# Performance work log

Hardware: AMD Instinct MI355X
Metric: run time of the kernel (lower is better)

## Reference

```python
import jax, jax.numpy as jnp
import numpy as np

G, N_NODES, E, H, D, IN_DIM, NS = 1024, 64, 128, 8, 32, 256, 48
EPS = 1e-6

def setup_inputs() -> dict:
    key = jax.random.key(0)
    ks = jax.random.split(key, 10)
    s = 1.0 / np.sqrt(IN_DIM)
    return {
        'h': jax.random.normal(ks[0], (G * N_NODES, IN_DIM), jnp.float32),
        'Wq': jax.random.normal(ks[1], (IN_DIM, H * D), jnp.float32) * s,
        'bq': jax.random.normal(ks[2], (H * D,), jnp.float32) * 0.01,
        'Wk': jax.random.normal(ks[3], (IN_DIM, H * D), jnp.float32) * s,
        'bk': jax.random.normal(ks[4], (H * D,), jnp.float32) * 0.01,
        'Wv': jax.random.normal(ks[5], (IN_DIM, H * D), jnp.float32) * s,
        'bv': jax.random.normal(ks[6], (H * D,), jnp.float32) * 0.01,
        'src': jax.random.randint(ks[7], (E,), 0, N_NODES, jnp.int32),
        'dst': jax.random.randint(ks[8], (E,), 0, N_NODES, jnp.int32),
        'ns': jax.random.randint(ks[9], (E, NS), 0, N_NODES, jnp.int32),
    }

def reference(h, Wq, bq, Wk, bk, Wv, bv, src, dst, ns):
    # per-node projections, reshaped per-graph: [G, n, H, D]
    Q = (h @ Wq + bq).reshape(G, N_NODES, H, D)
    K = (h @ Wk + bk).reshape(G, N_NODES, H, D)
    V = (h @ Wv + bv).reshape(G, N_NODES, H, D)
    # QK[g, s, h, t] = Q[g,s,h] . K[g,t,h], clamped as in torch .clamp(-5, 5)
    QK = jnp.clip(jnp.einsum('gshd,gthd->gsht', Q, K), -5.0, 5.0)  # [G, n, H, n]
    QKs = QK[:, src]  # rows for each edge's source node: [G, E, H, n]
    # numerator: QK[:, src_e, :, dst_e]
    num = jnp.take_along_axis(
        QKs, jnp.broadcast_to(dst[None, :, None, None].astype(jnp.int32), (G, E, H, 1)), axis=3
    )[..., 0]  # [G, E, H]
    # denominator: sum of QK[:, src_e, :, non_siblings(e)]
    den = jnp.take_along_axis(
        QKs, jnp.broadcast_to(ns[None, :, None, :], (G, E, H, NS)), axis=3
    ).sum(-1)  # [G, E, H]
    score = num / (den + EPS)  # [G, E, H]
    # scatter-sum aggregation: wV[g, dst] += V[g, src] * score; z[g, dst] += score
    msg = V[:, src] * score[..., None]  # [G, E, H, D]
    seg = (jnp.arange(G, dtype=jnp.int32)[:, None] * N_NODES + dst[None, :]).reshape(-1)
    wV = jax.ops.segment_sum(msg.reshape(G * E, H, D), seg, num_segments=G * N_NODES)
    z = jax.ops.segment_sum(score.reshape(G * E, H), seg, num_segments=G * N_NODES)
    return wV / (z[..., None] + EPS)  # [G*n, H, D]
```

## Files before the change

kernel.cpp:

```cpp
#include <hip/hip_runtime.h>

#define NG    1024
#define NN    64
#define NE    128
#define NH    8
#define ND    32
#define INDIM 256
#define NS_   48
#define EPS_  1e-6
#define BK    16

#define WS_QKV_FLOATS ((size_t)NG * NH * 3 * NN * ND)
#define WS_ELIST_OFF  (WS_QKV_FLOATS * sizeof(float))
#define WS_CNT_OFF    (WS_ELIST_OFF + (size_t)NN * 64 * sizeof(unsigned short))
#define WS_NEED2      (WS_CNT_OFF + (size_t)NN * sizeof(int))

__global__ __launch_bounds__(256, 2) void qkv_gemm_kernel(
    const float* __restrict__ h,
    const float* __restrict__ Wq, const float* __restrict__ bq,
    const float* __restrict__ Wk, const float* __restrict__ bk,
    const float* __restrict__ Wv, const float* __restrict__ bv,
    float* __restrict__ ws)
{
  const int b    = blockIdx.x;
  const int xcd  = b & 7;
  const int slot = b >> 3;
  const int rt   = xcd * 64 + slot / 3;
  const int sel  = slot % 3;
  const int tid  = threadIdx.x;

  const float* W  = (sel == 0) ? Wq : (sel == 1) ? Wk : Wv;
  const float* bs = (sel == 0) ? bq : (sel == 1) ? bk : bv;

  __shared__ float hT[BK][132];
  __shared__ float wT[BK][260];

  const int ty  = tid >> 5;
  const int tx  = tid & 31;
  const int r16 = ty * 16;
  const int ca  = tx * 4;
  const int cb  = 128 + tx * 4;

  float acc[16][8];
  #pragma unroll
  for (int i = 0; i < 16; ++i)
    #pragma unroll
    for (int j = 0; j < 8; ++j) acc[i][j] = 0.f;

  const int ra  = tid >> 1;
  const int kof = (tid & 1) * 8;
  const int kb2 = tid >> 6;
  const int c4  = (tid & 63) * 4;
  const float* hp0 = h + ((size_t)(rt * 128 + ra)) * INDIM + kof;
  const float* wp0 = W + (size_t)kb2 * (NH * ND) + c4;

  float4 pa0, pa1, pb[4];
  pa0 = *(const float4*)(hp0);
  pa1 = *(const float4*)(hp0 + 4);
  #pragma unroll
  for (int j = 0; j < 4; ++j)
    pb[j] = *(const float4*)(wp0 + (size_t)(4 * j) * (NH * ND));

  for (int kc = 0; kc < INDIM / BK; ++kc) {
    __syncthreads();
    hT[kof + 0][ra] = pa0.x; hT[kof + 1][ra] = pa0.y;
    hT[kof + 2][ra] = pa0.z; hT[kof + 3][ra] = pa0.w;
    hT[kof + 4][ra] = pa1.x; hT[kof + 5][ra] = pa1.y;
    hT[kof + 6][ra] = pa1.z; hT[kof + 7][ra] = pa1.w;
    #pragma unroll
    for (int j = 0; j < 4; ++j)
      *(float4*)&wT[kb2 + 4 * j][c4] = pb[j];
    __syncthreads();

    if (kc + 1 < INDIM / BK) {
      const int k0n = (kc + 1) * BK;
      pa0 = *(const float4*)(hp0 + k0n);
      pa1 = *(const float4*)(hp0 + k0n + 4);
      #pragma unroll
      for (int j = 0; j < 4; ++j)
        pb[j] = *(const float4*)(wp0 + (size_t)(k0n + 4 * j) * (NH * ND));
    }

    #pragma unroll
    for (int k = 0; k < BK; ++k) {
      float4 a0 = *(const float4*)&hT[k][r16];
      float4 a1 = *(const float4*)&hT[k][r16 + 4];
      float4 a2 = *(const float4*)&hT[k][r16 + 8];
      float4 a3 = *(const float4*)&hT[k][r16 + 12];
      float4 b0 = *(const float4*)&wT[k][ca];
      float4 b1 = *(const float4*)&wT[k][cb];
      const float av[16] = {a0.x,a0.y,a0.z,a0.w, a1.x,a1.y,a1.z,a1.w,
                            a2.x,a2.y,a2.z,a2.w, a3.x,a3.y,a3.z,a3.w};
      #pragma unroll
      for (int i = 0; i < 16; ++i) {
        acc[i][0] += av[i] * b0.x;
        acc[i][1] += av[i] * b0.y;
        acc[i][2] += av[i] * b0.z;
        acc[i][3] += av[i] * b0.w;
        acc[i][4] += av[i] * b1.x;
        acc[i][5] += av[i] * b1.y;
        acc[i][6] += av[i] * b1.z;
        acc[i][7] += av[i] * b1.w;
      }
    }
  }

  const int hda = ca >> 5, d0a = ca & 31;
  const int hdb = cb >> 5, d0b = cb & 31;
  float ba4[4], bb4[4];
  #pragma unroll
  for (int j = 0; j < 4; ++j) { ba4[j] = bs[ca + j]; bb4[j] = bs[cb + j]; }

  #pragma unroll
  for (int i = 0; i < 16; ++i) {
    const int r = rt * 128 + r16 + i;
    const int g = r >> 6, n = r & 63;
    float* opa = ws + ((((size_t)(g * NH + hda)) * 3 + sel) * NN + n) * ND + d0a;
    float* opb = ws + ((((size_t)(g * NH + hdb)) * 3 + sel) * NN + n) * ND + d0b;
    *(float4*)opa = make_float4(acc[i][0] + ba4[0], acc[i][1] + ba4[1],
                                acc[i][2] + ba4[2], acc[i][3] + ba4[3]);
    *(float4*)opb = make_float4(acc[i][4] + bb4[0], acc[i][5] + bb4[1],
                                acc[i][6] + bb4[2], acc[i][7] + bb4[3]);
  }
}

__global__ void edge_setup_kernel(const int* __restrict__ dst,
                                  unsigned short* __restrict__ elist,
                                  int* __restrict__ cnt)
{
  const int n = threadIdx.x;
  if (n < NN) {
    int c = 0;
    for (int e = 0; e < NE; ++e) {
      if (dst[e] == n) {
        if (c < 64) elist[n * 64 + c] = (unsigned short)e;
        ++c;
      }
    }
    cnt[n] = (c > 64) ? 64 : c;
  }
}

__global__ __launch_bounds__(256, 5) void attn_kernel(
    const float* __restrict__ ws,
    const int* __restrict__ src, const int* __restrict__ dst,
    const int* __restrict__ ns,
    const unsigned short* __restrict__ elist_g, const int* __restrict__ cnt_g,
    float* __restrict__ out)
{
  const int hd  = blockIdx.x;
  const int g   = blockIdx.y;
  const int tid = threadIdx.x;
  const int ty  = tid >> 4, tx = tid & 15;

  __shared__ union {
    struct { float QT[32][68]; float KT[32][68]; } a;
    float QK[64][65];
  } uQ;
  __shared__ float Vs[64][36];
  __shared__ float  score_s[NE];
  __shared__ int    srcs[NE], dsts[NE];
  __shared__ double z_s[NN];

  const float* base = ws + ((size_t)(g * NH + hd)) * 3 * (NN * ND);
  {
    const int nr = tid >> 3;
    const int d4 = (tid & 7) * 4;
    #pragma unroll
    for (int half = 0; half < 2; ++half) {
      const int n = half * 32 + nr;
      float4 q = *(const float4*)(base + (size_t)n * ND + d4);
      float4 k = *(const float4*)(base + (size_t)(NN * ND) + (size_t)n * ND + d4);
      float4 v = *(const float4*)(base + (size_t)(2 * NN * ND) + (size_t)n * ND + d4);
      uQ.a.QT[d4 + 0][n] = q.x; uQ.a.QT[d4 + 1][n] = q.y;
      uQ.a.QT[d4 + 2][n] = q.z; uQ.a.QT[d4 + 3][n] = q.w;
      uQ.a.KT[d4 + 0][n] = k.x; uQ.a.KT[d4 + 1][n] = k.y;
      uQ.a.KT[d4 + 2][n] = k.z; uQ.a.KT[d4 + 3][n] = k.w;
      *(float4*)&Vs[n][d4] = v;
    }
  }
  __syncthreads();

  {
    const int s0 = ty * 4, t0 = tx * 4;
    float qk[4][4];
    #pragma unroll
    for (int i = 0; i < 4; ++i)
      #pragma unroll
      for (int j = 0; j < 4; ++j) qk[i][j] = 0.f;
    #pragma unroll
    for (int k = 0; k < ND; ++k) {
      float4 qa = *(const float4*)&uQ.a.QT[k][s0];
      float4 kb = *(const float4*)&uQ.a.KT[k][t0];
      qk[0][0] += qa.x * kb.x; qk[0][1] += qa.x * kb.y; qk[0][2] += qa.x * kb.z; qk[0][3] += qa.x * kb.w;
      qk[1][0] += qa.y * kb.x; qk[1][1] += qa.y * kb.y; qk[1][2] += qa.y * kb.z; qk[1][3] += qa.y * kb.w;
      qk[2][0] += qa.z * kb.x; qk[2][1] += qa.z * kb.y; qk[2][2] += qa.z * kb.z; qk[2][3] += qa.z * kb.w;
      qk[3][0] += qa.w * kb.x; qk[3][1] += qa.w * kb.y; qk[3][2] += qa.w * kb.z; qk[3][3] += qa.w * kb.w;
    }
    __syncthreads();
    #pragma unroll
    for (int i = 0; i < 4; ++i)
      #pragma unroll
      for (int j = 0; j < 4; ++j) {
        float v = qk[i][j];
        v = fminf(5.f, fmaxf(-5.f, v));
        uQ.QK[s0 + i][t0 + j] = v;
      }
  }
  __syncthreads();

  if (tid < NE) {
    const int e = tid;
    const int s = src[e], dd = dst[e];
    srcs[e] = s; dsts[e] = dd;
    const float num = uQ.QK[s][dd];
    double den = 0.0;
    const int* np_ = ns + (size_t)e * NS_;
    #pragma unroll
    for (int j = 0; j < NS_; ++j) den += (double)uQ.QK[s][np_[j]];
    score_s[e] = (float)((double)num / (den + (double)EPS_));
  }
  __syncthreads();

  if (tid < NN) {
    const int cn = cnt_g[tid];
    double zz = 0.0;
    for (int c = 0; c < cn; ++c)
      zz += (double)score_s[elist_g[tid * 64 + c]];
    z_s[tid] = zz;
  }
  __syncthreads();

  {
    const int n  = tid >> 2;
    const int d0 = (tid & 3) * 8;
    float wvv[8];
    #pragma unroll
    for (int i = 0; i < 8; ++i) wvv[i] = 0.f;
    const int cn = cnt_g[n];
    for (int c = 0; c < cn; ++c) {
      const int e  = elist_g[n * 64 + c];
      const float sc = score_s[e];
      const int s  = srcs[e];
      float4 v0 = *(const float4*)&Vs[s][d0];
      float4 v1 = *(const float4*)&Vs[s][d0 + 4];
      wvv[0] += sc * v0.x; wvv[1] += sc * v0.y; wvv[2] += sc * v0.z; wvv[3] += sc * v0.w;
      wvv[4] += sc * v1.x; wvv[5] += sc * v1.y; wvv[6] += sc * v1.z; wvv[7] += sc * v1.w;
    }
    const double zz = z_s[n] + (double)EPS_;
    float o[8];
    #pragma unroll
    for (int i = 0; i < 8; ++i) o[i] = (float)((double)wvv[i] / zz);
    float* op = out + (((size_t)(g * NN + n)) * NH + hd) * ND + d0;
    *(float4*)(op)     = make_float4(o[0], o[1], o[2], o[3]);
    *(float4*)(op + 4) = make_float4(o[4], o[5], o[6], o[7]);
  }
}

__global__ __launch_bounds__(256, 4) void raal_fused_kernel(
    const float* __restrict__ h,
    const float* __restrict__ Wq, const float* __restrict__ bq,
    const float* __restrict__ Wk, const float* __restrict__ bk,
    const float* __restrict__ Wv, const float* __restrict__ bv,
    const int*   __restrict__ src, const int* __restrict__ dst,
    const int*   __restrict__ ns,
    float* __restrict__ out)
{
  const int hd  = blockIdx.x;
  const int g   = blockIdx.y;
  const int tid = threadIdx.x;
  const int ty  = tid >> 4, tx = tid & 15;

  __shared__ union {
    struct { float QT[32][64]; float KT[32][64]; } s2;
    float QK[64][64];
  } uQ;
  __shared__ float Vs[64][32];
  __shared__ union {
    struct { float hT[BK][68]; float wT[BK][100]; } s1;
    struct { float score[NE]; int srcs[NE]; int dsts[NE];
             double z[NN]; unsigned short elist[NN][64]; int cnt[NN]; } s3;
  } uA;

  const int r0 = ty * 4;
  const int c4 = tx * 4;
  const int cv = tx * 2;

  float accqk[4][4], accv[4][2];
  #pragma unroll
  for (int i = 0; i < 4; ++i) {
    #pragma unroll
    for (int j = 0; j < 4; ++j) accqk[i][j] = 0.f;
    accv[i][0] = 0.f; accv[i][1] = 0.f;
  }

  const int lr  = tid >> 2;
  const int lk4 = (tid & 3) * 4;
  const int wr  = ty;
  const int wc  = tx * 2;
  const float* hrow = h + ((size_t)(g * NN + lr)) * INDIM + lk4;
  const size_t wcol = (size_t)hd * ND + wc;

  float4 hv; float2 wq2, wk2, wv2;
  {
    hv  = *(const float4*)(hrow);
    const size_t wro = (size_t)wr * (NH * ND) + wcol;
    wq2 = *(const float2*)(Wq + wro);
    wk2 = *(const float2*)(Wk + wro);
    wv2 = *(const float2*)(Wv + wro);
  }

  for (int kc = 0; kc < INDIM / BK; ++kc) {
    __syncthreads();
    uA.s1.hT[lk4 + 0][lr] = hv.x;
    uA.s1.hT[lk4 + 1][lr] = hv.y;
    uA.s1.hT[lk4 + 2][lr] = hv.z;
    uA.s1.hT[lk4 + 3][lr] = hv.w;
    *(float2*)&uA.s1.wT[wr][ 0 + wc] = wq2;
    *(float2*)&uA.s1.wT[wr][32 + wc] = wk2;
    *(float2*)&uA.s1.wT[wr][64 + wc] = wv2;
    __syncthreads();

    if (kc + 1 < INDIM / BK) {
      const int k0n = (kc + 1) * BK;
      hv  = *(const float4*)(hrow + k0n);
      const size_t wro = (size_t)(k0n + wr) * (NH * ND) + wcol;
      wq2 = *(const float2*)(Wq + wro);
      wk2 = *(const float2*)(Wk + wro);
      wv2 = *(const float2*)(Wv + wro);
    }

    #pragma unroll
    for (int k = 0; k < BK; ++k) {
      float4 a  = *(const float4*)&uA.s1.hT[k][r0];
      float4 b  = *(const float4*)&uA.s1.wT[k][c4];
      float2 bv2 = *(const float2*)&uA.s1.wT[k][64 + cv];
      #pragma unroll
      for (int i = 0; i < 4; ++i) {
        const float ai = (i == 0) ? a.x : (i == 1) ? a.y : (i == 2) ? a.z : a.w;
        accqk[i][0] += ai * b.x;
        accqk[i][1] += ai * b.y;
        accqk[i][2] += ai * b.z;
        accqk[i][3] += ai * b.w;
        accv[i][0]  += ai * bv2.x;
        accv[i][1]  += ai * bv2.y;
      }
    }
  }

  {
    if (tx < 8) {
      #pragma unroll
      for (int j = 0; j < 4; ++j) {
        const int c = c4 + j;
        const float b = bq[hd * ND + c];
        #pragma unroll
        for (int i = 0; i < 4; ++i) uQ.s2.QT[c][r0 + i] = accqk[i][j] + b;
      }
    } else {
      #pragma unroll
      for (int j = 0; j < 4; ++j) {
        const int c = c4 - 32 + j;
        const float b = bk[hd * ND + c];
        #pragma unroll
        for (int i = 0; i < 4; ++i) uQ.s2.KT[c][r0 + i] = accqk[i][j] + b;
      }
    }
    const float b0 = bv[hd * ND + cv], b1 = bv[hd * ND + cv + 1];
    #pragma unroll
    for (int i = 0; i < 4; ++i) {
      Vs[r0 + i][cv]     = accv[i][0] + b0;
      Vs[r0 + i][cv + 1] = accv[i][1] + b1;
    }
  }
  __syncthreads();

  {
    const int s0 = ty * 4, t0 = tx * 4;
    float qk[4][4];
    #pragma unroll
    for (int i = 0; i < 4; ++i)
      #pragma unroll
      for (int j = 0; j < 4; ++j) qk[i][j] = 0.f;
    #pragma unroll
    for (int k = 0; k < ND; ++k) {
      float4 qa = *(const float4*)&uQ.s2.QT[k][s0];
      float4 kb = *(const float4*)&uQ.s2.KT[k][t0];
      qk[0][0] += qa.x * kb.x; qk[0][1] += qa.x * kb.y; qk[0][2] += qa.x * kb.z; qk[0][3] += qa.x * kb.w;
      qk[1][0] += qa.y * kb.x; qk[1][1] += qa.y * kb.y; qk[1][2] += qa.y * kb.z; qk[1][3] += qa.y * kb.w;
      qk[2][0] += qa.z * kb.x; qk[2][1] += qa.z * kb.y; qk[2][2] += qa.z * kb.z; qk[2][3] += qa.z * kb.w;
      qk[3][0] += qa.w * kb.x; qk[3][1] += qa.w * kb.y; qk[3][2] += qa.w * kb.z; qk[3][3] += qa.w * kb.w;
    }
    __syncthreads();
    #pragma unroll
    for (int i = 0; i < 4; ++i)
      #pragma unroll
      for (int j = 0; j < 4; ++j) {
        float v = qk[i][j];
        v = fminf(5.f, fmaxf(-5.f, v));
        uQ.QK[s0 + i][t0 + j] = v;
      }
  }
  __syncthreads();

  if (tid < NE) {
    const int e = tid;
    const int s = src[e], dd = dst[e];
    uA.s3.srcs[e] = s; uA.s3.dsts[e] = dd;
    const float num = uQ.QK[s][dd];
    double den = 0.0;
    const int* np_ = ns + (size_t)e * NS_;
    #pragma unroll
    for (int j = 0; j < NS_; ++j) den += (double)uQ.QK[s][np_[j]];
    uA.s3.score[e] = (float)((double)num / (den + (double)EPS_));
  }
  __syncthreads();

  if (tid < NN) {
    int c = 0; double zz = 0.0;
    for (int e = 0; e < NE; ++e) {
      if (uA.s3.dsts[e] == tid) {
        zz += (double)uA.s3.score[e];
        if (c < 64) uA.s3.elist[tid][c] = (unsigned short)e;
        ++c;
      }
    }
    uA.s3.cnt[tid] = (c > 64) ? 64 : c;
    uA.s3.z[tid]   = zz;
  }
  __syncthreads();

  {
    const int n  = tid >> 2;
    const int d0 = (tid & 3) * 8;
    float wvv[8];
    #pragma unroll
    for (int i = 0; i < 8; ++i) wvv[i] = 0.f;
    const int cn = uA.s3.cnt[n];
    for (int c = 0; c < cn; ++c) {
      const int e  = uA.s3.elist[n][c];
      const float sc = uA.s3.score[e];
      const int s  = uA.s3.srcs[e];
      float4 v0 = *(const float4*)&Vs[s][d0];
      float4 v1 = *(const float4*)&Vs[s][d0 + 4];
      wvv[0] += sc * v0.x; wvv[1] += sc * v0.y; wvv[2] += sc * v0.z; wvv[3] += sc * v0.w;
      wvv[4] += sc * v1.x; wvv[5] += sc * v1.y; wvv[6] += sc * v1.z; wvv[7] += sc * v1.w;
    }
    const double zz = uA.s3.z[n] + (double)EPS_;
    float o[8];
    #pragma unroll
    for (int i = 0; i < 8; ++i) o[i] = (float)((double)wvv[i] / zz);
    float* op = out + (((size_t)(g * NN + n)) * NH + hd) * ND + d0;
    *(float4*)(op)     = make_float4(o[0], o[1], o[2], o[3]);
    *(float4*)(op + 4) = make_float4(o[4], o[5], o[6], o[7]);
  }
}

extern "C" void kernel_launch(void* const* d_in, const int* in_sizes, int n_in,
                              void* d_out, int out_size, void* d_ws, size_t ws_size,
                              hipStream_t stream) {
  const float* h   = (const float*)d_in[0];
  const float* Wq  = (const float*)d_in[1];
  const float* bq  = (const float*)d_in[2];
  const float* Wk  = (const float*)d_in[3];
  const float* bk  = (const float*)d_in[4];
  const float* Wv  = (const float*)d_in[5];
  const float* bv  = (const float*)d_in[6];
  const int*   src = (const int*)d_in[7];
  const int*   dst = (const int*)d_in[8];
  const int*   ns  = (const int*)d_in[9];
  float* out = (float*)d_out;

  dim3 b(256, 1, 1);
  if (ws_size >= WS_NEED2) {
    float* ws = (float*)d_ws;
    unsigned short* elist = (unsigned short*)((char*)d_ws + WS_ELIST_OFF);
    int* cnt = (int*)((char*)d_ws + WS_CNT_OFF);

    hipLaunchKernelGGL(qkv_gemm_kernel, dim3(1536, 1, 1), b, 0, stream,
                       h, Wq, bq, Wk, bk, Wv, bv, ws);
    hipLaunchKernelGGL(edge_setup_kernel, dim3(1, 1, 1), dim3(64, 1, 1), 0, stream,
                       dst, elist, cnt);
    hipLaunchKernelGGL(attn_kernel, dim3(NH, NG, 1), b, 0, stream,
                       ws, src, dst, ns, elist, cnt, out);
  } else {
    hipLaunchKernelGGL(raal_fused_kernel, dim3(NH, NG, 1), b, 0, stream,
                       h, Wq, bq, Wk, bk, Wv, bv, src, dst, ns, out);
  }
}
```

Baseline: 537.7 us.

## Compute V projection with split-fp16 MFMA GEMM in separate kernel

Moves the V projection out of the FP32 SIMT GEMM into a new kernel. It splits h and Wv into high and low fp16 parts and accumulates three MFMA products to get near-fp32 accuracy. The goal is to cut the cost of one third of the projection GEMM by using matrix cores, while Q and K stay on the existing FP32 path. It adds a kernel launch, uncoalesced scalar output stores and strided per-column weight loads, and the split-fp16 scheme may lose some accuracy relative to fp32.

```diff
diff --git a/kernel.cpp b/kernel.cpp
--- a/kernel.cpp
+++ b/kernel.cpp
@@ -10,27 +10,34 @@
 #define EPS_  1e-6
 #define BK    16
 
+#define GBM   128
+#define GBN   128
+#define GBK   64
+
 #define WS_QKV_FLOATS ((size_t)NG * NH * 3 * NN * ND)
 #define WS_ELIST_OFF  (WS_QKV_FLOATS * sizeof(float))
 #define WS_CNT_OFF    (WS_ELIST_OFF + (size_t)NN * 64 * sizeof(unsigned short))
 #define WS_NEED2      (WS_CNT_OFF + (size_t)NN * sizeof(int))
 
+typedef _Float16 half8_t __attribute__((ext_vector_type(8)));
+typedef _Float16 half4_t __attribute__((ext_vector_type(4)));
+typedef float    f32x4_t __attribute__((ext_vector_type(4)));
+
 __global__ __launch_bounds__(256, 2) void qkv_gemm_kernel(
     const float* __restrict__ h,
     const float* __restrict__ Wq, const float* __restrict__ bq,
     const float* __restrict__ Wk, const float* __restrict__ bk,
-    const float* __restrict__ Wv, const float* __restrict__ bv,
     float* __restrict__ ws)
 {
   const int b    = blockIdx.x;
   const int xcd  = b & 7;
   const int slot = b >> 3;
-  const int rt   = xcd * 64 + slot / 3;
-  const int sel  = slot % 3;
+  const int rt   = xcd * 64 + (slot >> 1);
+  const int sel  = slot & 1;
   const int tid  = threadIdx.x;
 
-  const float* W  = (sel == 0) ? Wq : (sel == 1) ? Wk : Wv;
-  const float* bs = (sel == 0) ? bq : (sel == 1) ? bk : bv;
+  const float* W  = (sel == 0) ? Wq : Wk;
+  const float* bs = (sel == 0) ? bq : bk;
 
   __shared__ float hT[BK][132];
   __shared__ float wT[BK][260];
@@ -121,6 +128,145 @@
                                 acc[i][2] + ba4[2], acc[i][3] + ba4[3]);
     *(float4*)opb = make_float4(acc[i][4] + bb4[0], acc[i][5] + bb4[1],
                                 acc[i][6] + bb4[2], acc[i][7] + bb4[3]);
+  }
+}
+
+__device__ __forceinline__ void* swz_pt(void* base, int row, int k) {
+  size_t byte = ((size_t)(row * GBK + k)) * 2;
+  byte ^= (size_t)((row & 7) << 4);
+  return (void*)((char*)base + byte);
+}
+
+__global__ __launch_bounds__(256, 2) void v_gemm_mfma(
+    const float* __restrict__ h,
+    const float* __restrict__ Wv, const float* __restrict__ bv,
+    float* __restrict__ ws)
+{
+  const int b    = blockIdx.x;
+  const int xcd  = b & 7;
+  const int slot = b >> 3;
+  const int rt   = xcd * 64 + (slot >> 1);
+  const int ct   = slot & 1;
+
+  __shared__ __align__(16) _Float16 Ahh[GBM * GBK];
+  __shared__ __align__(16) _Float16 Ahl[GBM * GBK];
+  __shared__ __align__(16) _Float16 Bhh[GBN * GBK];
+  __shared__ __align__(16) _Float16 Bhl[GBN * GBK];
+
+  const int tid  = threadIdx.x;
+  const int lane = tid & 63;
+  const int wvid = tid >> 6;
+  const int wm   = wvid >> 1;
+  const int wn   = wvid & 1;
+  const int lr   = lane & 15;
+  const int lg   = lane >> 4;
+
+  f32x4_t acc0[4][4], acc1[4][4];
+  #pragma unroll
+  for (int i = 0; i < 4; ++i)
+    #pragma unroll
+    for (int j = 0; j < 4; ++j) {
+      acc0[i][j] = (f32x4_t){0.f, 0.f, 0.f, 0.f};
+      acc1[i][j] = (f32x4_t){0.f, 0.f, 0.f, 0.f};
+    }
+
+  const float* hA  = h + (size_t)rt * GBM * INDIM;
+  const int bnn    = tid >> 1;
+  const int bkh    = (tid & 1) * 32;
+  const int c0     = ct * GBN;
+  const float* wB  = Wv + (size_t)bkh * (NH * ND) + (c0 + bnn);
+
+  for (int kc = 0; kc < INDIM / GBK; ++kc) {
+    float4 av4[8];
+    #pragma unroll
+    for (int i = 0; i < 8; ++i) {
+      const int idx = i * 256 + tid;
+      const int row = idx >> 4, kq = idx & 15;
+      av4[i] = *(const float4*)(hA + (size_t)row * INDIM + kc * GBK + kq * 4);
+    }
+    float wv32[32];
+    #pragma unroll
+    for (int j = 0; j < 32; ++j)
+      wv32[j] = wB[(size_t)(kc * GBK + j) * (NH * ND)];
+
+    if (kc) __syncthreads();
+
+    #pragma unroll
+    for (int i = 0; i < 8; ++i) {
+      const int idx = i * 256 + tid;
+      const int row = idx >> 4, kq = idx & 15;
+      half4_t ph, pl;
+      ph[0] = (_Float16)av4[i].x; ph[1] = (_Float16)av4[i].y;
+      ph[2] = (_Float16)av4[i].z; ph[3] = (_Float16)av4[i].w;
+      pl[0] = (_Float16)((av4[i].x - (float)ph[0]) * 2048.f);
+      pl[1] = (_Float16)((av4[i].y - (float)ph[1]) * 2048.f);
+      pl[2] = (_Float16)((av4[i].z - (float)ph[2]) * 2048.f);
+      pl[3] = (_Float16)((av4[i].w - (float)ph[3]) * 2048.f);
+      *(half4_t*)swz_pt(Ahh, row, kq * 4) = ph;
+      *(half4_t*)swz_pt(Ahl, row, kq * 4) = pl;
+    }
+    #pragma unroll
+    for (int c = 0; c < 4; ++c) {
+      half8_t ph, pl;
+      #pragma unroll
+      for (int j = 0; j < 8; ++j) {
+        const float a  = wv32[c * 8 + j];
+        const _Float16 x = (_Float16)a;
+        ph[j] = x;
+        pl[j] = (_Float16)((a - (float)x) * 2048.f);
+      }
+      *(half8_t*)swz_pt(Bhh, bnn, bkh + c * 8) = ph;
+      *(half8_t*)swz_pt(Bhl, bnn, bkh + c * 8) = pl;
+    }
+    __syncthreads();
+
+    #pragma unroll
+    for (int ks = 0; ks < 2; ++ks) {
+      const int kb = ks * 32 + lg * 8;
+      half8_t bh[4], bl[4];
+      #pragma unroll
+      for (int j = 0; j < 4; ++j) {
+        const int colr = wn * 64 + j * 16 + lr;
+        bh[j] = *(const half8_t*)swz_pt(Bhh, colr, kb);
+        bl[j] = *(const half8_t*)swz_pt(Bhl, colr, kb);
+      }
+      #pragma unroll
+      for (int i = 0; i < 4; ++i) {
+        const int rowr = wm * 64 + i * 16 + lr;
+        const half8_t ah = *(const half8_t*)swz_pt(Ahh, rowr, kb);
+        const half8_t al = *(const half8_t*)swz_pt(Ahl, rowr, kb);
+        #pragma unroll
+        for (int j = 0; j < 4; ++j) {
+          acc0[i][j] = __builtin_amdgcn_mfma_f32_16x16x32_f16(
+              ah, bh[j], acc0[i][j], 0, 0, 0);
+          acc1[i][j] = __builtin_amdgcn_mfma_f32_16x16x32_f16(
+              ah, bl[j], acc1[i][j], 0, 0, 0);
+          acc1[i][j] = __builtin_amdgcn_mfma_f32_16x16x32_f16(
+              al, bh[j], acc1[i][j], 0, 0, 0);
+        }
+      }
+    }
+  }
+
+  float bj[4];
+  #pragma unroll
+  for (int j = 0; j < 4; ++j) bj[j] = bv[c0 + wn * 64 + j * 16 + lr];
+
+  #pragma unroll
+  for (int i = 0; i < 4; ++i) {
+    #pragma unroll
+    for (int r = 0; r < 4; ++r) {
+      const int R = rt * GBM + wm * 64 + i * 16 + lg * 4 + r;
+      const int g = R >> 6, n = R & 63;
+      #pragma unroll
+      for (int j = 0; j < 4; ++j) {
+        const int col = c0 + wn * 64 + j * 16 + lr;
+        const int hd = col >> 5, d = col & 31;
+        const float val = acc0[i][j][r] + acc1[i][j][r] * (1.0f / 2048.0f)
+                          + bj[j];
+        ws[((((size_t)(g * NH + hd)) * 3 + 2) * NN + n) * ND + d] = val;
+      }
+    }
   }
 }
 
@@ -477,8 +623,10 @@
     unsigned short* elist = (unsigned short*)((char*)d_ws + WS_ELIST_OFF);
     int* cnt = (int*)((char*)d_ws + WS_CNT_OFF);
 
-    hipLaunchKernelGGL(qkv_gemm_kernel, dim3(1536, 1, 1), b, 0, stream,
-                       h, Wq, bq, Wk, bk, Wv, bv, ws);
+    hipLaunchKernelGGL(qkv_gemm_kernel, dim3(1024, 1, 1), b, 0, stream,
+                       h, Wq, bq, Wk, bk, ws);
+    hipLaunchKernelGGL(v_gemm_mfma, dim3(1024, 1, 1), b, 0, stream,
+                       h, Wv, bv, ws);
     hipLaunchKernelGGL(edge_setup_kernel, dim3(1, 1, 1), dim3(64, 1, 1), 0, stream,
                        dst, elist, cnt);
     hipLaunchKernelGGL(attn_kernel, dim3(NH, NG, 1), b, 0, stream,
```

Result: faster. 498.7 us (-7.3%).
